# Kernel optimization log

Hardware: AMD Instinct MI355X
Metric: run time of the kernel (lower is better)

The kernel has to match this reference:

```python
import jax, jax.numpy as jnp
import numpy as np

EMBED_DIM = 768
NUM_HEADS = 12
HEAD_DIM = EMBED_DIM // NUM_HEADS


def setup_inputs() -> dict:
    key = jax.random.key(0)
    ks = jax.random.split(key, 9)
    B, N, D = 8, 1024, EMBED_DIM
    s = 1.0 / np.sqrt(D)
    x = jax.random.normal(ks[0], (B, N, D), dtype=jnp.float32)
    Wq = jax.random.normal(ks[1], (D, D), dtype=jnp.float32) * s
    bq = jnp.zeros((D,), dtype=jnp.float32)
    Wk = jax.random.normal(ks[2], (D, D), dtype=jnp.float32) * s
    bk = jnp.zeros((D,), dtype=jnp.float32)
    Wv = jax.random.normal(ks[3], (D, D), dtype=jnp.float32) * s
    bv = jnp.zeros((D,), dtype=jnp.float32)
    Wo = jax.random.normal(ks[4], (D, D), dtype=jnp.float32) * s
    bo = jnp.zeros((D,), dtype=jnp.float32)
    return {"x": x, "Wq": Wq, "bq": bq, "Wk": Wk, "bk": bk,
            "Wv": Wv, "bv": bv, "Wo": Wo, "bo": bo}


def reference(x, Wq, bq, Wk, bk, Wv, bv, Wo, bo):
    B, N, D = x.shape
    H, Hd = NUM_HEADS, HEAD_DIM
    # torch Linear: y = x @ W.T + b
    q = (x @ Wq.T + bq).reshape(B, N, H, Hd).transpose(0, 2, 1, 3)  # [B,H,N,Hd]
    k = (x @ Wk.T + bk).reshape(B, N, H, Hd).transpose(0, 2, 1, 3)
    v = (x @ Wv.T + bv).reshape(B, N, H, Hd).transpose(0, 2, 1, 3)
    # NOTE: original scales by embed_dim**-0.5 (not head_dim)
    scale = jnp.asarray(D, x.dtype) ** -0.5
    scores = jnp.einsum('bhnd,bhmd->bhnm', q, k) * scale  # [B,H,N,N]
    attn = jax.nn.softmax(scores, axis=-1)
    out = jnp.einsum('bhnm,bhmd->bhnd', attn, v)  # dropout: identity in eval
    out = out.transpose(0, 2, 1, 3).reshape(B, N, D)
    return out @ Wo.T + bo
```

## Files before the change

kernel.cpp:

```cpp
#include <hip/hip_runtime.h>
#include <math.h>


typedef __bf16 bf16x8 __attribute__((ext_vector_type(8)));
typedef float  f32x4  __attribute__((ext_vector_type(4)));
typedef unsigned u32x2 __attribute__((ext_vector_type(2)));
typedef unsigned u32x4 __attribute__((ext_vector_type(4)));
typedef unsigned short ushort_t;

__device__ __forceinline__ unsigned short f2bf(float f) {
    unsigned u = __float_as_uint(f);
    u += 0x7fffu + ((u >> 16) & 1u);
    return (unsigned short)(u >> 16);
}
__device__ __forceinline__ unsigned pk16(unsigned short lo, unsigned short hi) {
    return (unsigned)lo | ((unsigned)hi << 16);
}

#define GLL16(g, l)                                                                        \
    __builtin_amdgcn_global_load_lds((const __attribute__((address_space(1))) void*)(g),   \
                                     (__attribute__((address_space(3))) void*)(l), 16, 0, 0)

__global__ __launch_bounds__(256)
void cast_all(const float* __restrict__ x,
              const float* __restrict__ w0, const float* __restrict__ w1,
              const float* __restrict__ w2, const float* __restrict__ w3,
              ushort_t* __restrict__ xb, ushort_t* __restrict__ wb0,
              ushort_t* __restrict__ wb1, ushort_t* __restrict__ wb2,
              ushort_t* __restrict__ wb3)
{
    const int bid = blockIdx.x;
    if (bid < 3072) {
        const int i = (bid * 256 + threadIdx.x) * 8;
        const float4 f0 = *(const float4*)(x + i);
        const float4 f1 = *(const float4*)(x + i + 4);
        ushort4 p0, p1;
        p0.x = f2bf(f0.x); p0.y = f2bf(f0.y); p0.z = f2bf(f0.z); p0.w = f2bf(f0.w);
        p1.x = f2bf(f1.x); p1.y = f2bf(f1.y); p1.z = f2bf(f1.z); p1.w = f2bf(f1.w);
        *(ushort4*)(xb + i)     = p0;
        *(ushort4*)(xb + i + 4) = p1;
        return;
    }
    const int wt = (bid - 3072) * 4 + (threadIdx.x >> 6);
    const int wsel = wt / 1152, tile = wt % 1152;
    const float* s; ushort_t* d;
    switch (wsel) {
        case 0:  s = w0; d = wb0; break;
        case 1:  s = w1; d = wb1; break;
        case 2:  s = w2; d = wb2; break;
        default: s = w3; d = wb3; break;
    }
    const int t = tile / 24, kb = tile % 24;
    const int L = threadIdx.x & 63, c = L & 15, g = L >> 4;
    const float* sp = s + (size_t)(t * 16 + c) * 768 + kb * 32 + g * 8;
    const float4 f0 = *(const float4*)sp;
    const float4 f1 = *(const float4*)(sp + 4);
    ushort4 p0, p1;
    p0.x = f2bf(f0.x); p0.y = f2bf(f0.y); p0.z = f2bf(f0.z); p0.w = f2bf(f0.w);
    p1.x = f2bf(f1.x); p1.y = f2bf(f1.y); p1.z = f2bf(f1.z); p1.w = f2bf(f1.w);
    ushort_t* dp = d + ((size_t)tile * 64 + L) * 8;
    *(ushort4*)dp       = p0;
    *(ushort4*)(dp + 4) = p1;
}

__global__ __launch_bounds__(256, 3)
void gemm_qkv(const ushort_t* __restrict__ xb,
              const ushort_t* __restrict__ wqb, const ushort_t* __restrict__ wkb,
              const ushort_t* __restrict__ wvb,
              const float* __restrict__ bq, const float* __restrict__ bk,
              const float* __restrict__ bv,
              ushort_t* __restrict__ Qh, ushort_t* __restrict__ Kl,
              ushort_t* __restrict__ Vl)
{
    __shared__ ushort_t smem[9216];
    ushort_t* As = smem;

    const int tid = threadIdx.x, L = tid & 63, wv = tid >> 6;
    const int c = L & 15, g = L >> 4;
    const int n0 = blockIdx.x * 128, m0 = blockIdx.y * 64;

    const int qs = ((tid & 3) ^ ((tid >> 3) & 3)) * 8;
    const ushort_t* ap = xb + (size_t)(m0 + (tid >> 2)) * 768 + qs;
    const int sg = (g ^ ((c >> 1) & 3)) * 8;

    const size_t wbase = ((size_t)(blockIdx.x * 8 + wv * 2) * 24 * 64 + L) * 8;
    const ushort_t* wqp = wqb + wbase;
    const ushort_t* wkp = wkb + wbase;
    const ushort_t* wvp = wvb + wbase;

    f32x4 acc[3][4][2];
#pragma unroll
    for (int z = 0; z < 3; ++z)
#pragma unroll
        for (int i = 0; i < 4; ++i)
#pragma unroll
            for (int j = 0; j < 2; ++j) acc[z][i][j] = (f32x4){0.f, 0.f, 0.f, 0.f};

    GLL16(ap, &As[(size_t)tid * 8]);
    __builtin_amdgcn_sched_barrier(0);

    bf16x8 wf[3][2];
#pragma unroll
    for (int j = 0; j < 2; ++j) {
        wf[0][j] = *(const bf16x8*)(wqp + j * 12288);
        wf[1][j] = *(const bf16x8*)(wkp + j * 12288);
        wf[2][j] = *(const bf16x8*)(wvp + j * 12288);
    }

    for (int kb = 0; kb < 24; ++kb) {
        asm volatile("s_waitcnt vmcnt(6) lgkmcnt(0)" ::: "memory");
        __builtin_amdgcn_s_barrier();
        __builtin_amdgcn_sched_barrier(0);
        if (kb < 23) {
            GLL16(ap + (kb + 1) * 32,
                  &As[((kb + 1) & 1) * 2048 + (size_t)tid * 8]);
            __builtin_amdgcn_sched_barrier(0);
        }
        const ushort_t* Ab = &As[(kb & 1) * 2048];
        bf16x8 af[4];
#pragma unroll
        for (int i = 0; i < 4; ++i)
            af[i] = *(const bf16x8*)&Ab[(i * 16 + c) * 32 + sg];
#pragma unroll
        for (int z = 0; z < 3; ++z)
#pragma unroll
            for (int i = 0; i < 4; ++i)
#pragma unroll
                for (int j = 0; j < 2; ++j)
                    acc[z][i][j] = __builtin_amdgcn_mfma_f32_16x16x32_bf16(
                        af[i], wf[z][j], acc[z][i][j], 0, 0, 0);
        const int kn = (kb < 23) ? kb + 1 : 23;
#pragma unroll
        for (int j = 0; j < 2; ++j) {
            wf[0][j] = *(const bf16x8*)(wqp + j * 12288 + kn * 512);
            wf[1][j] = *(const bf16x8*)(wkp + j * 12288 + kn * 512);
            wf[2][j] = *(const bf16x8*)(wvp + j * 12288 + kn * 512);
        }
    }

    const int b  = m0 >> 10, nb = m0 & 1023;
    const int hcol = n0 + wv * 32;
    const int h = hcol >> 6, uh = (hcol >> 5) & 1;
    const int bh = b * 12 + h;
    ushort_t* scr = smem + wv * 2304;

    float bias2[3][2];
#pragma unroll
    for (int j = 0; j < 2; ++j) {
        bias2[0][j] = bq[hcol + j * 16 + c];
        bias2[1][j] = bk[hcol + j * 16 + c];
        bias2[2][j] = bv[hcol + j * 16 + c];
    }

    __syncthreads();

#pragma unroll
    for (int i = 0; i < 4; ++i)
#pragma unroll
        for (int j = 0; j < 2; ++j)
#pragma unroll
            for (int r = 0; r < 4; ++r)
                scr[(i * 16 + g * 4 + r) * 36 + j * 16 + c] =
                    f2bf(acc[0][i][j][r] + bias2[0][j]);
#pragma unroll
    for (int e = 0; e < 4; ++e) {
        const int slot = e * 64 + L;
        const int row = slot >> 2, ch = slot & 3;
        const u32x4 v = *(const u32x4*)&scr[row * 36 + ch * 8];
        *(u32x4*)&Qh[((size_t)bh * 1024 + nb + row) * 64 + uh * 32 + ch * 8] = v;
    }

#pragma unroll
    for (int i = 0; i < 4; ++i)
#pragma unroll
        for (int j = 0; j < 2; ++j)
#pragma unroll
            for (int r = 0; r < 4; ++r)
                scr[(i * 16 + g * 4 + r) * 36 + j * 16 + c] =
                    f2bf(acc[1][i][j][r] + bias2[1][j]);
#pragma unroll
    for (int tau = 0; tau < 4; ++tau) {
        const u32x4 v = *(const u32x4*)&scr[(tau * 16 + c) * 36 + g * 8];
        *(u32x4*)&Kl[(((size_t)bh * 64 + (nb >> 4) + tau) * 2 + uh) * 512
                     + (size_t)L * 8] = v;
    }

#pragma unroll
    for (int i = 0; i < 4; ++i)
#pragma unroll
        for (int j = 0; j < 2; ++j)
#pragma unroll
            for (int r = 0; r < 4; ++r)
                scr[(j * 16 + c) * 68 + i * 16 + g * 4 + r] =
                    f2bf(acc[2][i][j][r] + bias2[2][j]);
    const int T = nb >> 6;
#pragma unroll
    for (int t = 0; t < 4; ++t) {
        const int htl = t >> 1, u = t & 1;
        const u32x4 v = *(const u32x4*)&scr[(htl * 16 + c) * 68 + u * 32 + g * 8];
        *(u32x4*)&Vl[((((size_t)bh * 4 + uh * 2 + htl) * 16 + T) * 2 + u) * 512
                     + (size_t)L * 8] = v;
    }
}

__global__ __launch_bounds__(256, 3)
void gemm_outp(const ushort_t* __restrict__ attnb, const ushort_t* __restrict__ wob,
               const float* __restrict__ bo, float* __restrict__ out)
{
    __shared__ ushort_t smem[4096];
    ushort_t* As = smem;
    const int tid = threadIdx.x, L = tid & 63, wv = tid >> 6;
    const int c = L & 15, g = L >> 4;
    const int n0 = blockIdx.x * 128, m0 = blockIdx.y * 64;
    const int qs = ((tid & 3) ^ ((tid >> 3) & 3)) * 8;
    const ushort_t* ap = attnb + (size_t)(m0 + (tid >> 2)) * 768 + qs;
    const int sg = (g ^ ((c >> 1) & 3)) * 8;

    const size_t wbase = ((size_t)(blockIdx.x * 8 + wv * 2) * 24 * 64 + L) * 8;
    const ushort_t* wop = wob + wbase;

    f32x4 acc[4][2];
#pragma unroll
    for (int i = 0; i < 4; ++i)
#pragma unroll
        for (int j = 0; j < 2; ++j) acc[i][j] = (f32x4){0.f, 0.f, 0.f, 0.f};

    GLL16(ap, &As[(size_t)tid * 8]);
    __builtin_amdgcn_sched_barrier(0);

    bf16x8 wf[2];
#pragma unroll
    for (int j = 0; j < 2; ++j) wf[j] = *(const bf16x8*)(wop + j * 12288);

    for (int kb = 0; kb < 24; ++kb) {
        asm volatile("s_waitcnt vmcnt(2) lgkmcnt(0)" ::: "memory");
        __builtin_amdgcn_s_barrier();
        __builtin_amdgcn_sched_barrier(0);
        if (kb < 23) {
            GLL16(ap + (kb + 1) * 32,
                  &As[((kb + 1) & 1) * 2048 + (size_t)tid * 8]);
            __builtin_amdgcn_sched_barrier(0);
        }
        const ushort_t* Ab = &As[(kb & 1) * 2048];
        bf16x8 af[4];
#pragma unroll
        for (int i = 0; i < 4; ++i)
            af[i] = *(const bf16x8*)&Ab[(i * 16 + c) * 32 + sg];
#pragma unroll
        for (int i = 0; i < 4; ++i)
#pragma unroll
            for (int j = 0; j < 2; ++j)
                acc[i][j] = __builtin_amdgcn_mfma_f32_16x16x32_bf16(
                    af[i], wf[j], acc[i][j], 0, 0, 0);
        const int kn = (kb < 23) ? kb + 1 : 23;
#pragma unroll
        for (int j = 0; j < 2; ++j)
            wf[j] = *(const bf16x8*)(wop + j * 12288 + kn * 512);
    }

#pragma unroll
    for (int i = 0; i < 4; ++i) {
        const int row = m0 + i * 16 + g * 4;
#pragma unroll
        for (int j = 0; j < 2; ++j) {
            const int col = n0 + wv * 32 + j * 16 + c;
            const float bsvo = bo[col];
#pragma unroll
            for (int r = 0; r < 4; ++r)
                out[(size_t)(row + r) * 768 + col] = acc[i][j][r] + bsvo;
        }
    }
}

__global__ __launch_bounds__(64, 3)
void flash_bf16(const ushort_t* __restrict__ Q, const ushort_t* __restrict__ Kl,
                const ushort_t* __restrict__ Vl, ushort_t* __restrict__ attnb)
{
    __shared__ ushort_t Ps[2][2][16 * 68];
    const int L = threadIdx.x;
    const int c = L & 15, g = L >> 4;
    const int bid = blockIdx.x;
    const int slot = bid >> 3;
    const int bh = (bid & 7) * 12 + (slot >> 5);
    const int q0 = (slot & 31) * 32;
    const float SC2 = 0.05205954985329743f;

    const ushort_t* Qp = Q + ((size_t)bh * 1024 + q0 + c) * 64 + g * 8;
    bf16x8 qf[2][2];
    qf[0][0] = *(const bf16x8*)Qp;
    qf[0][1] = *(const bf16x8*)(Qp + 32);
    qf[1][0] = *(const bf16x8*)(Qp + 16 * 64);
    qf[1][1] = *(const bf16x8*)(Qp + 16 * 64 + 32);

    const ushort_t* Kb = Kl + (size_t)bh * 65536 + (size_t)L * 8;
    const ushort_t* Vb = Vl + (size_t)bh * 65536 + (size_t)L * 8;

    f32x4 o[2][4];
#pragma unroll
    for (int w = 0; w < 2; ++w)
#pragma unroll
        for (int ht = 0; ht < 4; ++ht) o[w][ht] = (f32x4){0.f, 0.f, 0.f, 0.f};
    float ls[2] = {0.f, 0.f};

    bf16x8 kf0[4], kf1[4];
#pragma unroll
    for (int ct = 0; ct < 4; ++ct) {
        kf0[ct] = *(const bf16x8*)(Kb + (size_t)(ct * 2 + 0) * 512);
        kf1[ct] = *(const bf16x8*)(Kb + (size_t)(ct * 2 + 1) * 512);
    }

    for (int T0 = 0; T0 < 16; T0 += 2) {
#pragma unroll
        for (int p = 0; p < 2; ++p) {
            const int T = T0 + p;
            bf16x8 vf0[4], vf1[4];
#pragma unroll
            for (int ht = 0; ht < 4; ++ht) {
                const ushort_t* vp = Vb + (size_t)((ht * 16 + T) * 2) * 512;
                vf0[ht] = *(const bf16x8*)vp;
                vf1[ht] = *(const bf16x8*)(vp + 512);
            }
            f32x4 s[2][4];
#pragma unroll
            for (int w = 0; w < 2; ++w)
#pragma unroll
                for (int ct = 0; ct < 4; ++ct) {
                    f32x4 zz = (f32x4){0.f, 0.f, 0.f, 0.f};
                    zz = __builtin_amdgcn_mfma_f32_16x16x32_bf16(kf0[ct], qf[w][0], zz, 0, 0, 0);
                    zz = __builtin_amdgcn_mfma_f32_16x16x32_bf16(kf1[ct], qf[w][1], zz, 0, 0, 0);
                    s[w][ct] = zz;
                }
            const int Tn = (T < 15) ? T + 1 : 15;
#pragma unroll
            for (int ct = 0; ct < 4; ++ct) {
                const ushort_t* kp = Kb + (size_t)((Tn * 4 + ct) * 2) * 512;
                kf0[ct] = *(const bf16x8*)kp;
                kf1[ct] = *(const bf16x8*)(kp + 512);
            }
#pragma unroll
            for (int w = 0; w < 2; ++w) {
#pragma unroll
                for (int ct = 0; ct < 4; ++ct) {
                    float pv[4];
#pragma unroll
                    for (int r = 0; r < 4; ++r)
                        pv[r] = __builtin_amdgcn_exp2f(s[w][ct][r] * SC2);
                    ls[w] += (pv[0] + pv[1]) + (pv[2] + pv[3]);
                    const unsigned w01 = __builtin_amdgcn_perm(
                        __float_as_uint(pv[1]), __float_as_uint(pv[0]), 0x07060302u);
                    const unsigned w23 = __builtin_amdgcn_perm(
                        __float_as_uint(pv[3]), __float_as_uint(pv[2]), 0x07060302u);
                    *(u32x2*)&Ps[p][w][c * 68 + ct * 16 + g * 4] = (u32x2){w01, w23};
                }
            }
#pragma unroll
            for (int w = 0; w < 2; ++w) {
                const int pb = c * 68 + g * 8;
                const u32x4 pa  = *(const u32x4*)&Ps[p][w][pb];
                const u32x4 pbv = *(const u32x4*)&Ps[p][w][pb + 32];
                const bf16x8 pf0 = __builtin_bit_cast(bf16x8, pa);
                const bf16x8 pf1 = __builtin_bit_cast(bf16x8, pbv);
#pragma unroll
                for (int ht = 0; ht < 4; ++ht) {
                    o[w][ht] = __builtin_amdgcn_mfma_f32_16x16x32_bf16(vf0[ht], pf0, o[w][ht], 0, 0, 0);
                    o[w][ht] = __builtin_amdgcn_mfma_f32_16x16x32_bf16(vf1[ht], pf1, o[w][ht], 0, 0, 0);
                }
            }
        }
    }

    const int b = bh / 12, h = bh % 12;
#pragma unroll
    for (int w = 0; w < 2; ++w) {
        float l = ls[w];
        l += __shfl_xor(l, 16);
        l += __shfl_xor(l, 32);
        const float inv = 1.f / l;
#pragma unroll
        for (int ht = 0; ht < 4; ++ht) {
            const unsigned w0 = pk16(f2bf(o[w][ht][0] * inv), f2bf(o[w][ht][1] * inv));
            const unsigned w1 = pk16(f2bf(o[w][ht][2] * inv), f2bf(o[w][ht][3] * inv));
            *(u32x2*)&Ps[0][w][c * 68 + ht * 16 + g * 4] = (u32x2){w0, w1};
        }
#pragma unroll
        for (int e = 0; e < 2; ++e) {
            const int row = e * 8 + (L >> 3);
            const int ch  = L & 7;
            const int si  = row * 68 + ch * 8;
            const u32x2 t0 = *(const u32x2*)&Ps[0][w][si];
            const u32x2 t1 = *(const u32x2*)&Ps[0][w][si + 4];
            *(u32x4*)&attnb[((size_t)(b * 1024 + q0 + w * 16 + row)) * 768 + h * 64 + ch * 8]
                = (u32x4){t0.x, t0.y, t1.x, t1.y};
        }
    }
}

extern "C" void kernel_launch(void* const* d_in, const int* in_sizes, int n_in,
                              void* d_out, int out_size, void* d_ws, size_t ws_size,
                              hipStream_t stream)
{
    const float* x  = (const float*)d_in[0];
    const float* Wq = (const float*)d_in[1];
    const float* bq = (const float*)d_in[2];
    const float* Wk = (const float*)d_in[3];
    const float* bk = (const float*)d_in[4];
    const float* Wv = (const float*)d_in[5];
    const float* bv = (const float*)d_in[6];
    const float* Wo = (const float*)d_in[7];
    const float* bo = (const float*)d_in[8];
    float* out = (float*)d_out;

    char* ws = (char*)d_ws;
    ushort_t* xb    = (ushort_t*)(ws);
    ushort_t* wqb   = (ushort_t*)(ws + 12582912);
    ushort_t* wkb   = (ushort_t*)(ws + 12582912 + 1179648);
    ushort_t* wvb   = (ushort_t*)(ws + 12582912 + 2359296);
    ushort_t* wob   = (ushort_t*)(ws + 12582912 + 3538944);
    ushort_t* Qh    = (ushort_t*)(ws + 17301504);
    ushort_t* Kl    = (ushort_t*)(ws + 29884416);
    ushort_t* Vl    = (ushort_t*)(ws + 42467328);
    ushort_t* attnb = (ushort_t*)(ws + 55050240);

    cast_all<<<dim3(4224), 256, 0, stream>>>(x, Wq, Wk, Wv, Wo,
                                             xb, wqb, wkb, wvb, wob);
    gemm_qkv<<<dim3(6, 128), 256, 0, stream>>>(xb, wqb, wkb, wvb,
                                               bq, bk, bv, Qh, Kl, Vl);
    flash_bf16<<<dim3(3072), 64, 0, stream>>>(Qh, Kl, Vl, attnb);
    gemm_outp<<<dim3(6, 128), 256, 0, stream>>>(attnb, wob, bo, out);
}
```

Measured before the change: 185.6 us.

## Store activations in MFMA fragment-tiled layout and load A operands directly to registers

The cast kernel now writes x in the same 16x32 fragment-tiled layout already used for the weights, and the attention kernel writes its output in that layout too. Both GEMMs then load A fragments straight from global memory into registers, like the weights, instead of staging them through LDS with global_load_lds, barriers and swizzled reads. This removes LDS traffic and per-iteration workgroup barriers. The cost is that each wave now issues its own global loads for A, so the four waves read the same A data redundantly and latency hiding depends on the register prefetch.

After: 183.1 us. No clear change (-1.4%).

```diff
diff --git a/kernel.cpp b/kernel.cpp
--- a/kernel.cpp
+++ b/kernel.cpp
@@ -16,10 +16,6 @@
 __device__ __forceinline__ unsigned pk16(unsigned short lo, unsigned short hi) {
     return (unsigned)lo | ((unsigned)hi << 16);
 }
-
-#define GLL16(g, l)                                                                        \
-    __builtin_amdgcn_global_load_lds((const __attribute__((address_space(1))) void*)(g),   \
-                                     (__attribute__((address_space(3))) void*)(l), 16, 0, 0)
 
 __global__ __launch_bounds__(256)
 void cast_all(const float* __restrict__ x,
@@ -29,29 +25,22 @@
               ushort_t* __restrict__ wb1, ushort_t* __restrict__ wb2,
               ushort_t* __restrict__ wb3)
 {
-    const int bid = blockIdx.x;
-    if (bid < 3072) {
-        const int i = (bid * 256 + threadIdx.x) * 8;
-        const float4 f0 = *(const float4*)(x + i);
-        const float4 f1 = *(const float4*)(x + i + 4);
-        ushort4 p0, p1;
-        p0.x = f2bf(f0.x); p0.y = f2bf(f0.y); p0.z = f2bf(f0.z); p0.w = f2bf(f0.w);
-        p1.x = f2bf(f1.x); p1.y = f2bf(f1.y); p1.z = f2bf(f1.z); p1.w = f2bf(f1.w);
-        *(ushort4*)(xb + i)     = p0;
-        *(ushort4*)(xb + i + 4) = p1;
-        return;
-    }
-    const int wt = (bid - 3072) * 4 + (threadIdx.x >> 6);
-    const int wsel = wt / 1152, tile = wt % 1152;
-    const float* s; ushort_t* d;
-    switch (wsel) {
-        case 0:  s = w0; d = wb0; break;
-        case 1:  s = w1; d = wb1; break;
-        case 2:  s = w2; d = wb2; break;
-        default: s = w3; d = wb3; break;
+    const int wt0 = blockIdx.x * 4 + (threadIdx.x >> 6);
+    const int L = threadIdx.x & 63, c = L & 15, g = L >> 4;
+    const float* s; ushort_t* d; int tile;
+    if (wt0 < 12288) {
+        s = x; d = xb; tile = wt0;
+    } else {
+        const int wt = wt0 - 12288;
+        const int wsel = wt / 1152; tile = wt % 1152;
+        switch (wsel) {
+            case 0:  s = w0; d = wb0; break;
+            case 1:  s = w1; d = wb1; break;
+            case 2:  s = w2; d = wb2; break;
+            default: s = w3; d = wb3; break;
+        }
     }
     const int t = tile / 24, kb = tile % 24;
-    const int L = threadIdx.x & 63, c = L & 15, g = L >> 4;
     const float* sp = s + (size_t)(t * 16 + c) * 768 + kb * 32 + g * 8;
     const float4 f0 = *(const float4*)sp;
     const float4 f1 = *(const float4*)(sp + 4);
@@ -73,16 +62,11 @@
               ushort_t* __restrict__ Vl)
 {
     __shared__ ushort_t smem[9216];
-    ushort_t* As = smem;
-
     const int tid = threadIdx.x, L = tid & 63, wv = tid >> 6;
     const int c = L & 15, g = L >> 4;
     const int n0 = blockIdx.x * 128, m0 = blockIdx.y * 64;
 
-    const int qs = ((tid & 3) ^ ((tid >> 3) & 3)) * 8;
-    const ushort_t* ap = xb + (size_t)(m0 + (tid >> 2)) * 768 + qs;
-    const int sg = (g ^ ((c >> 1) & 3)) * 8;
-
+    const ushort_t* ap = xb + (size_t)(blockIdx.y * 4) * 24 * 512 + (size_t)L * 8;
     const size_t wbase = ((size_t)(blockIdx.x * 8 + wv * 2) * 24 * 64 + L) * 8;
     const ushort_t* wqp = wqb + wbase;
     const ushort_t* wkp = wkb + wbase;
@@ -96,10 +80,9 @@
 #pragma unroll
             for (int j = 0; j < 2; ++j) acc[z][i][j] = (f32x4){0.f, 0.f, 0.f, 0.f};
 
-    GLL16(ap, &As[(size_t)tid * 8]);
-    __builtin_amdgcn_sched_barrier(0);
-
-    bf16x8 wf[3][2];
+    bf16x8 af[4], wf[3][2];
+#pragma unroll
+    for (int i = 0; i < 4; ++i) af[i] = *(const bf16x8*)(ap + i * 12288);
 #pragma unroll
     for (int j = 0; j < 2; ++j) {
         wf[0][j] = *(const bf16x8*)(wqp + j * 12288);
@@ -108,19 +91,6 @@
     }
 
     for (int kb = 0; kb < 24; ++kb) {
-        asm volatile("s_waitcnt vmcnt(6) lgkmcnt(0)" ::: "memory");
-        __builtin_amdgcn_s_barrier();
-        __builtin_amdgcn_sched_barrier(0);
-        if (kb < 23) {
-            GLL16(ap + (kb + 1) * 32,
-                  &As[((kb + 1) & 1) * 2048 + (size_t)tid * 8]);
-            __builtin_amdgcn_sched_barrier(0);
-        }
-        const ushort_t* Ab = &As[(kb & 1) * 2048];
-        bf16x8 af[4];
-#pragma unroll
-        for (int i = 0; i < 4; ++i)
-            af[i] = *(const bf16x8*)&Ab[(i * 16 + c) * 32 + sg];
 #pragma unroll
         for (int z = 0; z < 3; ++z)
 #pragma unroll
@@ -130,6 +100,9 @@
                     acc[z][i][j] = __builtin_amdgcn_mfma_f32_16x16x32_bf16(
                         af[i], wf[z][j], acc[z][i][j], 0, 0, 0);
         const int kn = (kb < 23) ? kb + 1 : 23;
+#pragma unroll
+        for (int i = 0; i < 4; ++i)
+            af[i] = *(const bf16x8*)(ap + i * 12288 + kn * 512);
 #pragma unroll
         for (int j = 0; j < 2; ++j) {
             wf[0][j] = *(const bf16x8*)(wqp + j * 12288 + kn * 512);
@@ -152,8 +125,6 @@
         bias2[2][j] = bv[hcol + j * 16 + c];
     }
 
-    __syncthreads();
-
 #pragma unroll
     for (int i = 0; i < 4; ++i)
 #pragma unroll
@@ -207,15 +178,11 @@
 void gemm_outp(const ushort_t* __restrict__ attnb, const ushort_t* __restrict__ wob,
                const float* __restrict__ bo, float* __restrict__ out)
 {
-    __shared__ ushort_t smem[4096];
-    ushort_t* As = smem;
     const int tid = threadIdx.x, L = tid & 63, wv = tid >> 6;
     const int c = L & 15, g = L >> 4;
     const int n0 = blockIdx.x * 128, m0 = blockIdx.y * 64;
-    const int qs = ((tid & 3) ^ ((tid >> 3) & 3)) * 8;
-    const ushort_t* ap = attnb + (size_t)(m0 + (tid >> 2)) * 768 + qs;
-    const int sg = (g ^ ((c >> 1) & 3)) * 8;
-
+
+    const ushort_t* ap = attnb + (size_t)(blockIdx.y * 4) * 24 * 512 + (size_t)L * 8;
     const size_t wbase = ((size_t)(blockIdx.x * 8 + wv * 2) * 24 * 64 + L) * 8;
     const ushort_t* wop = wob + wbase;
 
@@ -225,27 +192,13 @@
 #pragma unroll
         for (int j = 0; j < 2; ++j) acc[i][j] = (f32x4){0.f, 0.f, 0.f, 0.f};
 
-    GLL16(ap, &As[(size_t)tid * 8]);
-    __builtin_amdgcn_sched_barrier(0);
-
-    bf16x8 wf[2];
+    bf16x8 af[4], wf[2];
+#pragma unroll
+    for (int i = 0; i < 4; ++i) af[i] = *(const bf16x8*)(ap + i * 12288);
 #pragma unroll
     for (int j = 0; j < 2; ++j) wf[j] = *(const bf16x8*)(wop + j * 12288);
 
     for (int kb = 0; kb < 24; ++kb) {
-        asm volatile("s_waitcnt vmcnt(2) lgkmcnt(0)" ::: "memory");
-        __builtin_amdgcn_s_barrier();
-        __builtin_amdgcn_sched_barrier(0);
-        if (kb < 23) {
-            GLL16(ap + (kb + 1) * 32,
-                  &As[((kb + 1) & 1) * 2048 + (size_t)tid * 8]);
-            __builtin_amdgcn_sched_barrier(0);
-        }
-        const ushort_t* Ab = &As[(kb & 1) * 2048];
-        bf16x8 af[4];
-#pragma unroll
-        for (int i = 0; i < 4; ++i)
-            af[i] = *(const bf16x8*)&Ab[(i * 16 + c) * 32 + sg];
 #pragma unroll
         for (int i = 0; i < 4; ++i)
 #pragma unroll
@@ -253,6 +206,9 @@
                 acc[i][j] = __builtin_amdgcn_mfma_f32_16x16x32_bf16(
                     af[i], wf[j], acc[i][j], 0, 0, 0);
         const int kn = (kb < 23) ? kb + 1 : 23;
+#pragma unroll
+        for (int i = 0; i < 4; ++i)
+            af[i] = *(const bf16x8*)(ap + i * 12288 + kn * 512);
 #pragma unroll
         for (int j = 0; j < 2; ++j)
             wf[j] = *(const bf16x8*)(wop + j * 12288 + kn * 512);
@@ -370,6 +326,7 @@
     }
 
     const int b = bh / 12, h = bh % 12;
+    const int tB = b * 64 + (q0 >> 4);
 #pragma unroll
     for (int w = 0; w < 2; ++w) {
         float l = ls[w];
@@ -383,14 +340,9 @@
             *(u32x2*)&Ps[0][w][c * 68 + ht * 16 + g * 4] = (u32x2){w0, w1};
         }
 #pragma unroll
-        for (int e = 0; e < 2; ++e) {
-            const int row = e * 8 + (L >> 3);
-            const int ch  = L & 7;
-            const int si  = row * 68 + ch * 8;
-            const u32x2 t0 = *(const u32x2*)&Ps[0][w][si];
-            const u32x2 t1 = *(const u32x2*)&Ps[0][w][si + 4];
-            *(u32x4*)&attnb[((size_t)(b * 1024 + q0 + w * 16 + row)) * 768 + h * 64 + ch * 8]
-                = (u32x4){t0.x, t0.y, t1.x, t1.y};
+        for (int kbi = 0; kbi < 2; ++kbi) {
+            const u32x4 v = *(const u32x4*)&Ps[0][w][c * 68 + kbi * 32 + g * 8];
+            *(u32x4*)&attnb[(((size_t)(tB + w) * 24 + h * 2 + kbi) * 64 + L) * 8] = v;
         }
     }
 }
```
